# Optimization experiments

Measured on AMD Instinct MI355X. Metric: run time of the kernel, lower is better.

The kernel has to match this reference:

```python
import jax, jax.numpy as jnp
import numpy as np

# Grouped masked GEMM dims (see DeepSeekMOE._up_gate/_down):
# G = num_experts // ep = 8; M = m_per_group = 32
# up/gate: k = hidden_size = 4096, n = 2*expert_dim = 2816
# down   : k = expert_dim  = 1408, n = hidden_size = 4096
G, M = 8, 32
K_UG, N_UG = 4096, 2816
K_DN, N_DN = 1408, 4096


def setup_inputs() -> dict:
    key = jax.random.key(0)
    k1, k2, k3, k4, k5 = jax.random.split(key, 5)
    x_ug = jax.random.normal(k1, (G, M, K_UG), dtype=jnp.float32)
    w_ug = jax.random.normal(k2, (G, N_UG, K_UG), dtype=jnp.float32) * 0.02  # NT layout [g, n, k]
    x_dn = jax.random.normal(k3, (G, M, K_DN), dtype=jnp.float32)
    w_dn = jax.random.normal(k4, (G, N_DN, K_DN), dtype=jnp.float32) * 0.02  # NT layout [g, n, k]
    masked_m = jax.random.randint(k5, (G,), 0, M, dtype=jnp.int32)  # per-group valid row count
    return {"x_ug": x_ug, "w_ug": w_ug, "x_dn": x_dn, "w_dn": w_dn, "masked_m": masked_m}


def reference(x_ug, w_ug, x_dn, w_dn, masked_m):
    # Row-validity mask: rows >= masked_m[g] are skipped by the masked grouped GEMM
    # (their output is zero / undefined; we define it as zero).
    row = jnp.arange(M, dtype=jnp.int32)
    mask = (row[None, :] < masked_m[:, None])[:, :, None]  # [G, M, 1]

    # Masked grouped GEMM, NT layout: out[g] = x[g] @ w[g].T on valid rows.
    out_ug = jnp.einsum('gmk,gnk->gmn', x_ug, w_ug)  # [G, M, N_UG]  up/gate proj
    out_dn = jnp.einsum('gmk,gnk->gmn', x_dn, w_dn)  # [G, M, N_DN]  down proj

    out_ug = jnp.where(mask, out_ug, jnp.zeros((), out_ug.dtype))
    out_dn = jnp.where(mask, out_dn, jnp.zeros((), out_dn.dtype))
    # Pack both grouped-GEMM outputs into one array along the feature dim.
    return jnp.concatenate([out_ug, out_dn], axis=-1)  # [G, M, N_UG + N_DN]
```

## Files before the change

### kernel.cpp

```cpp
#include <hip/hip_runtime.h>
#include <hip/hip_bf16.h>


#define G_    8
#define M_    32
#define KUG   4096
#define NUG   2816
#define KDN   1408
#define NDN   4096
#define NOUT  (NUG + NDN)
#define BN    32
#define BK    128
#define UPT   (NUG / BN)
#define DNT   (NDN / BN)
#define UPG   (UPT + DNT)
#define XUG_E (G_ * M_ * KUG)
#define XDN_E (G_ * M_ * KDN)
#define XBF_BYTES ((size_t)(XUG_E + XDN_E) * 2)

typedef __attribute__((ext_vector_type(8))) short bf16x8;
typedef __attribute__((ext_vector_type(4))) float f32x4;

typedef __attribute__((address_space(3))) float        lds_f32;
typedef const __attribute__((address_space(1))) float  gbl_f32;

__device__ __forceinline__ short f2bf(float x) {
  union { __hip_bfloat16 h; short s; } u;
  u.h = __hip_bfloat16(x);
  return u.s;
}
__device__ __forceinline__ bf16x8 cvt8(f32x4 lo, f32x4 hi) {
  bf16x8 o;
#pragma unroll
  for (int j = 0; j < 4; ++j) { o[j] = f2bf(lo[j]); o[4 + j] = f2bf(hi[j]); }
  return o;
}

__global__ void cvt_x_kernel(const float* __restrict__ xu, const float* __restrict__ xd,
                             short* __restrict__ du, short* __restrict__ dd) {
  int i = blockIdx.x * 256 + threadIdx.x;
  const float* s; short* d;
  int j = i;
  if (i < XUG_E / 8) { s = xu; d = du; }
  else { s = xd; d = dd; j = i - XUG_E / 8; if (j >= XDN_E / 8) return; }
  f32x4 lo = *(const f32x4*)(s + (size_t)j * 8);
  f32x4 hi = *(const f32x4*)(s + (size_t)j * 8 + 4);
  *(bf16x8*)(d + (size_t)j * 8) = cvt8(lo, hi);
}

__device__ __forceinline__ void stageW(const float* wg, float* wbuf, int K,
                                       int k0, int t) {
#pragma unroll
  for (int i = 0; i < 16; ++i) {
    int gid = i * 64 + t;
    int row = gid >> 5;
    int q   = gid & 31;
    int qs  = q ^ (row & 7);
    __builtin_amdgcn_global_load_lds(
        (gbl_f32*)(wg + (size_t)row * K + k0 + qs * 4),
        (lds_f32*)(wbuf + gid * 4), 16, 0, 0);
  }
}

template<bool XBF>
__global__ __launch_bounds__(64, 2) void moe_masked_gemm(
    const float* __restrict__ x_ug, const float* __restrict__ w_ug,
    const float* __restrict__ x_dn, const float* __restrict__ w_dn,
    const short* __restrict__ xbf_ug, const short* __restrict__ xbf_dn,
    const int* __restrict__ masked_m, float* __restrict__ out) {
  __shared__ float wbuf[BN * BK];

  int b = blockIdx.x;
  int g = b & 7;
  int u = b >> 3;

  const float* wg;
  const float* xf;
  const short* xq;
  int K, NIT, n0, colOff;
  bool is_up = (u < UPT);
  if (is_up) {
    K = KUG; NIT = KUG / BK; n0 = u * BN; colOff = 0;
    wg = w_ug + ((size_t)g * NUG + n0) * KUG;
    xf = x_ug + (size_t)g * M_ * KUG;
    xq = xbf_ug + (size_t)g * M_ * KUG;
  } else {
    int d = u - UPT;
    K = KDN; NIT = KDN / BK; n0 = d * BN; colOff = NUG;
    wg = w_dn + ((size_t)g * NDN + n0) * KDN;
    xf = x_dn + (size_t)g * M_ * KDN;
    xq = xbf_dn + (size_t)g * M_ * KDN;
  }

  int mm = masked_m[g];
  int t  = threadIdx.x;
  int r  = t & 15, q4 = t >> 4;
  int sk = r & 7;

  f32x4 acc[2][2];
#pragma unroll
  for (int mf = 0; mf < 2; ++mf)
#pragma unroll
    for (int nf = 0; nf < 2; ++nf) acc[mf][nf] = (f32x4){0.f, 0.f, 0.f, 0.f};

  if (mm != 0) {
    for (int it = 0; it < NIT; ++it) {
      int k0 = it * BK;

      stageW(wg, wbuf, K, k0, t);

      bf16x8 xb[2][4];
      if constexpr (XBF) {
#pragma unroll
        for (int mf = 0; mf < 2; ++mf)
#pragma unroll
          for (int ks = 0; ks < 4; ++ks)
            xb[mf][ks] = *(const bf16x8*)(xq + (size_t)(mf * 16 + r) * K +
                                          k0 + ks * 32 + q4 * 8);
      } else {
#pragma unroll
        for (int mf = 0; mf < 2; ++mf)
#pragma unroll
          for (int ks = 0; ks < 4; ++ks) {
            const float* xp = xf + (size_t)(mf * 16 + r) * K + k0 + ks * 32 + q4 * 8;
            xb[mf][ks] = cvt8(*(const f32x4*)xp, *(const f32x4*)(xp + 4));
          }
      }

      asm volatile("s_waitcnt vmcnt(0)" ::: "memory");
      __builtin_amdgcn_sched_barrier(0);

#pragma unroll
      for (int ks = 0; ks < 4; ++ks) {
        int g0 = (ks * 4 + q4) * 2;
        int o0 = ((g0 ^ sk) << 2), o1 = (((g0 + 1) ^ sk) << 2);
#pragma unroll
        for (int nf = 0; nf < 2; ++nf) {
          const float* rowp = wbuf + (size_t)(nf * 16 + r) * BK;
          bf16x8 bb = cvt8(*(const f32x4*)(rowp + o0), *(const f32x4*)(rowp + o1));
          acc[0][nf] = __builtin_amdgcn_mfma_f32_16x16x32_bf16(xb[0][ks], bb, acc[0][nf], 0, 0, 0);
          acc[1][nf] = __builtin_amdgcn_mfma_f32_16x16x32_bf16(xb[1][ks], bb, acc[1][nf], 0, 0, 0);
        }
      }
    }
  }

  float* outg = out + (size_t)g * M_ * NOUT + colOff + n0;
#pragma unroll
  for (int i = 0; i < 4; ++i) {
    int m0 = q4 * 4 + i, m1 = 16 + m0;
    bool v0 = m0 < mm, v1 = m1 < mm;
#pragma unroll
    for (int nf = 0; nf < 2; ++nf) {
      outg[(size_t)m0 * NOUT + nf * 16 + r] = v0 ? acc[0][nf][i] : 0.f;
      outg[(size_t)m1 * NOUT + nf * 16 + r] = v1 ? acc[1][nf][i] : 0.f;
    }
  }
}

extern "C" void kernel_launch(void* const* d_in, const int* in_sizes, int n_in,
                              void* d_out, int out_size, void* d_ws, size_t ws_size,
                              hipStream_t stream) {
  const float* x_ug     = (const float*)d_in[0];
  const float* w_ug     = (const float*)d_in[1];
  const float* x_dn     = (const float*)d_in[2];
  const float* w_dn     = (const float*)d_in[3];
  const int*   masked_m = (const int*)d_in[4];
  float*       out      = (float*)d_out;

  short* xbf_ug = (short*)d_ws;
  short* xbf_dn = xbf_ug + XUG_E;

  if (ws_size >= XBF_BYTES) {
    int n8 = (XUG_E + XDN_E) / 8;
    cvt_x_kernel<<<dim3((n8 + 255) / 256), dim3(256), 0, stream>>>(
        x_ug, x_dn, xbf_ug, xbf_dn);
    moe_masked_gemm<true><<<dim3(G_ * UPG), dim3(64), 0, stream>>>(
        x_ug, w_ug, x_dn, w_dn, xbf_ug, xbf_dn, masked_m, out);
  } else {
    moe_masked_gemm<false><<<dim3(G_ * UPG), dim3(64), 0, stream>>>(
        x_ug, w_ug, x_dn, w_dn, xbf_ug, xbf_dn, masked_m, out);
  }
}
```

Baseline: 113.4 us.

## Widen N tile to 64 with two waves sharing LDS-staged bf16 activations

```diff
diff --git a/kernel.cpp b/kernel.cpp
--- a/kernel.cpp
+++ b/kernel.cpp
@@ -9,7 +9,7 @@
 #define KDN   1408
 #define NDN   4096
 #define NOUT  (NUG + NDN)
-#define BN    32
+#define BN    64
 #define BK    128
 #define UPT   (NUG / BN)
 #define DNT   (NDN / BN)
@@ -48,53 +48,39 @@
   *(bf16x8*)(d + (size_t)j * 8) = cvt8(lo, hi);
 }
 
-__device__ __forceinline__ void stageW(const float* wg, float* wbuf, int K,
-                                       int k0, int t) {
-#pragma unroll
-  for (int i = 0; i < 16; ++i) {
-    int gid = i * 64 + t;
-    int row = gid >> 5;
-    int q   = gid & 31;
-    int qs  = q ^ (row & 7);
-    __builtin_amdgcn_global_load_lds(
-        (gbl_f32*)(wg + (size_t)row * K + k0 + qs * 4),
-        (lds_f32*)(wbuf + gid * 4), 16, 0, 0);
-  }
-}
-
-template<bool XBF>
-__global__ __launch_bounds__(64, 2) void moe_masked_gemm(
-    const float* __restrict__ x_ug, const float* __restrict__ w_ug,
-    const float* __restrict__ x_dn, const float* __restrict__ w_dn,
+__global__ __launch_bounds__(128, 2) void moe_masked_gemm_bf(
+    const float* __restrict__ w_ug, const float* __restrict__ w_dn,
     const short* __restrict__ xbf_ug, const short* __restrict__ xbf_dn,
     const int* __restrict__ masked_m, float* __restrict__ out) {
-  __shared__ float wbuf[BN * BK];
+  __shared__ __attribute__((aligned(16))) float wbuf[64 * BK];
+  __shared__ __attribute__((aligned(16))) short xsh[32 * BK];
 
   int b = blockIdx.x;
   int g = b & 7;
-  int u = b >> 3;
+  int v = b >> 3;
+  int p = v / 27, s = v - p * 27;
+  int ub = (s * 11 + 16) / 27;
+  bool is_up = ((s * 11) % 27) < 11;
 
   const float* wg;
-  const float* xf;
   const short* xq;
   int K, NIT, n0, colOff;
-  bool is_up = (u < UPT);
   if (is_up) {
+    int u = p * 11 + ub;
     K = KUG; NIT = KUG / BK; n0 = u * BN; colOff = 0;
     wg = w_ug + ((size_t)g * NUG + n0) * KUG;
-    xf = x_ug + (size_t)g * M_ * KUG;
     xq = xbf_ug + (size_t)g * M_ * KUG;
   } else {
-    int d = u - UPT;
+    int d = p * 16 + (s - ub);
     K = KDN; NIT = KDN / BK; n0 = d * BN; colOff = NUG;
     wg = w_dn + ((size_t)g * NDN + n0) * KDN;
-    xf = x_dn + (size_t)g * M_ * KDN;
     xq = xbf_dn + (size_t)g * M_ * KDN;
   }
 
   int mm = masked_m[g];
   int t  = threadIdx.x;
-  int r  = t & 15, q4 = t >> 4;
+  int w  = t >> 6;
+  int r  = t & 15, q4 = (t >> 4) & 3;
   int sk = r & 7;
 
   f32x4 acc[2][2];
@@ -107,29 +93,105 @@
     for (int it = 0; it < NIT; ++it) {
       int k0 = it * BK;
 
-      stageW(wg, wbuf, K, k0, t);
+#pragma unroll
+      for (int i = 0; i < 16; ++i) {
+        int gid = i * 128 + t;
+        int row = gid >> 5, q = gid & 31, qs = q ^ (row & 7);
+        __builtin_amdgcn_global_load_lds(
+            (gbl_f32*)(wg + (size_t)row * K + k0 + qs * 4),
+            (lds_f32*)(wbuf + gid * 4), 16, 0, 0);
+      }
+#pragma unroll
+      for (int i = 0; i < 4; ++i) {
+        int gid = i * 128 + t;
+        int row = gid >> 4, q = gid & 15, qs = q ^ (row & 7);
+        __builtin_amdgcn_global_load_lds(
+            (gbl_f32*)(const void*)(xq + (size_t)row * K + k0 + qs * 8),
+            (lds_f32*)(void*)(xsh + gid * 8), 16, 0, 0);
+      }
+
+      __syncthreads();
 
       bf16x8 xb[2][4];
-      if constexpr (XBF) {
-#pragma unroll
-        for (int mf = 0; mf < 2; ++mf)
-#pragma unroll
-          for (int ks = 0; ks < 4; ++ks)
-            xb[mf][ks] = *(const bf16x8*)(xq + (size_t)(mf * 16 + r) * K +
-                                          k0 + ks * 32 + q4 * 8);
-      } else {
-#pragma unroll
-        for (int mf = 0; mf < 2; ++mf)
-#pragma unroll
-          for (int ks = 0; ks < 4; ++ks) {
-            const float* xp = xf + (size_t)(mf * 16 + r) * K + k0 + ks * 32 + q4 * 8;
-            xb[mf][ks] = cvt8(*(const f32x4*)xp, *(const f32x4*)(xp + 4));
-          }
-      }
-
+#pragma unroll
+      for (int mf = 0; mf < 2; ++mf)
+#pragma unroll
+        for (int ks = 0; ks < 4; ++ks) {
+          int phys = (ks * 4 + q4) ^ sk;
+          xb[mf][ks] = *(const bf16x8*)(xsh + (mf * 16 + r) * BK + phys * 8);
+        }
+
+#pragma unroll
+      for (int ks = 0; ks < 4; ++ks) {
+        int g0 = (ks * 4 + q4) * 2;
+        int o0 = ((g0 ^ sk) << 2), o1 = (((g0 + 1) ^ sk) << 2);
+#pragma unroll
+        for (int nf = 0; nf < 2; ++nf) {
+          const float* rowp = wbuf + (size_t)(w * 32 + nf * 16 + r) * BK;
+          bf16x8 bb = cvt8(*(const f32x4*)(rowp + o0), *(const f32x4*)(rowp + o1));
+          acc[0][nf] = __builtin_amdgcn_mfma_f32_16x16x32_bf16(xb[0][ks], bb, acc[0][nf], 0, 0, 0);
+          acc[1][nf] = __builtin_amdgcn_mfma_f32_16x16x32_bf16(xb[1][ks], bb, acc[1][nf], 0, 0, 0);
+        }
+      }
+
+      __syncthreads();
+    }
+  }
+
+  float* outg = out + (size_t)g * M_ * NOUT + colOff + n0 + w * 32;
+#pragma unroll
+  for (int i = 0; i < 4; ++i) {
+    int m0 = q4 * 4 + i, m1 = 16 + m0;
+    bool v0 = m0 < mm, v1 = m1 < mm;
+#pragma unroll
+    for (int nf = 0; nf < 2; ++nf) {
+      outg[(size_t)m0 * NOUT + nf * 16 + r] = v0 ? acc[0][nf][i] : 0.f;
+      outg[(size_t)m1 * NOUT + nf * 16 + r] = v1 ? acc[1][nf][i] : 0.f;
+    }
+  }
+}
+
+#define BN2   32
+#define UPT2  (NUG / BN2)
+#define UPG2  (UPT2 + NDN / BN2)
+__global__ __launch_bounds__(64, 2) void moe_masked_gemm_f32(
+    const float* __restrict__ x_ug, const float* __restrict__ w_ug,
+    const float* __restrict__ x_dn, const float* __restrict__ w_dn,
+    const int* __restrict__ masked_m, float* __restrict__ out) {
+  __shared__ float wbuf[BN2 * BK];
+  int b = blockIdx.x, g = b & 7, u = b >> 3;
+  const float* wg; const float* xf;
+  int K, NIT, n0, colOff;
+  bool is_up = (u < UPT2);
+  if (is_up) { K = KUG; NIT = KUG / BK; n0 = u * BN2; colOff = 0;
+    wg = w_ug + ((size_t)g * NUG + n0) * KUG; xf = x_ug + (size_t)g * M_ * KUG;
+  } else { int d = u - UPT2; K = KDN; NIT = KDN / BK; n0 = d * BN2; colOff = NUG;
+    wg = w_dn + ((size_t)g * NDN + n0) * KDN; xf = x_dn + (size_t)g * M_ * KDN; }
+  int mm = masked_m[g], t = threadIdx.x, r = t & 15, q4 = t >> 4, sk = r & 7;
+  f32x4 acc[2][2];
+#pragma unroll
+  for (int mf = 0; mf < 2; ++mf)
+#pragma unroll
+    for (int nf = 0; nf < 2; ++nf) acc[mf][nf] = (f32x4){0.f, 0.f, 0.f, 0.f};
+  if (mm != 0) {
+    for (int it = 0; it < NIT; ++it) {
+      int k0 = it * BK;
+#pragma unroll
+      for (int i = 0; i < 16; ++i) {
+        int gid = i * 64 + t, row = gid >> 5, q = gid & 31, qs = q ^ (row & 7);
+        __builtin_amdgcn_global_load_lds((gbl_f32*)(wg + (size_t)row * K + k0 + qs * 4),
+                                         (lds_f32*)(wbuf + gid * 4), 16, 0, 0);
+      }
+      bf16x8 xb[2][4];
+#pragma unroll
+      for (int mf = 0; mf < 2; ++mf)
+#pragma unroll
+        for (int ks = 0; ks < 4; ++ks) {
+          const float* xp = xf + (size_t)(mf * 16 + r) * K + k0 + ks * 32 + q4 * 8;
+          xb[mf][ks] = cvt8(*(const f32x4*)xp, *(const f32x4*)(xp + 4));
+        }
       asm volatile("s_waitcnt vmcnt(0)" ::: "memory");
       __builtin_amdgcn_sched_barrier(0);
-
 #pragma unroll
       for (int ks = 0; ks < 4; ++ks) {
         int g0 = (ks * 4 + q4) * 2;
@@ -144,7 +206,6 @@
       }
     }
   }
-
   float* outg = out + (size_t)g * M_ * NOUT + colOff + n0;
 #pragma unroll
   for (int i = 0; i < 4; ++i) {
@@ -175,10 +236,10 @@
     int n8 = (XUG_E + XDN_E) / 8;
     cvt_x_kernel<<<dim3((n8 + 255) / 256), dim3(256), 0, stream>>>(
         x_ug, x_dn, xbf_ug, xbf_dn);
-    moe_masked_gemm<true><<<dim3(G_ * UPG), dim3(64), 0, stream>>>(
-        x_ug, w_ug, x_dn, w_dn, xbf_ug, xbf_dn, masked_m, out);
+    moe_masked_gemm_bf<<<dim3(G_ * UPG), dim3(128), 0, stream>>>(
+        w_ug, w_dn, xbf_ug, xbf_dn, masked_m, out);
   } else {
-    moe_masked_gemm<false><<<dim3(G_ * UPG), dim3(64), 0, stream>>>(
-        x_ug, w_ug, x_dn, w_dn, xbf_ug, xbf_dn, masked_m, out);
-  }
-}
+    moe_masked_gemm_f32<<<dim3(G_ * UPG2), dim3(64), 0, stream>>>(
+        x_ug, w_ug, x_dn, w_dn, masked_m, out);
+  }
+}
```

After: 143.3 us. 1.26x slower.
